# Performance work log

Hardware: AMD Instinct MI355X
Metric: run time of the kernel (lower is better)

Reference implementation:

```python
import jax, jax.numpy as jnp
import numpy as np

BINS = 10

def setup_inputs() -> dict:
    key = jax.random.key(0)
    k1, k2 = jax.random.split(key)
    N, C = 262144, 80
    pred = jax.random.normal(k1, (N, C), dtype=jnp.float32)
    target = jax.random.randint(k2, (N, C), 0, 2, dtype=jnp.int32)
    return {"pred": pred, "target": target}


def _ghmc_loss(pred, target):
    # NOTE: faithful to the original torch code, which applies sigmoid to pred
    # and then feeds that *through binary_cross_entropy_with_logits* (i.e. the
    # sigmoid output is treated as logits -- a double sigmoid quirk we preserve).
    z = jax.nn.sigmoid(pred)                      # [N, C] "logits" fed to BCE-with-logits
    t = target.astype(z.dtype)                    # [N, C]
    # gradient magnitude, detached like pred.detach() in torch
    g = jnp.abs(jax.lax.stop_gradient(z) - t)     # in [0, 1]
    # label_weight is overwritten with ones in the original forward, so every
    # element is valid: tot = N * C.
    tot = jnp.asarray(z.size, dtype=z.dtype)

    # uniform bins: edges[i] = i/BINS, last edge nudged by 1e-6 so g == 1 lands
    # in the last bin -> equivalent to floor(g*BINS) clipped to BINS-1.
    idx = jnp.clip((g * BINS).astype(jnp.int32), 0, BINS - 1)   # [N, C]
    counts = jax.ops.segment_sum(
        jnp.ones((z.size,), dtype=z.dtype), idx.reshape(-1), num_segments=BINS
    )                                                            # [BINS]
    n_nonempty = jnp.sum(counts > 0).astype(z.dtype)
    per_bin_w = jnp.where(counts > 0, tot / jnp.maximum(counts, 1.0), 0.0)  # [BINS]
    weights = per_bin_w[idx] / jnp.maximum(n_nonempty, 1.0)      # [N, C]
    weights = jax.lax.stop_gradient(weights)

    # BCE-with-logits(z, t) = softplus(z) - t*z (numerically stable)
    bce = jax.nn.softplus(z) - t * z
    return jnp.sum(weights * bce) / tot


def reference(pred, target):
    return _ghmc_loss(pred, target)
```

## Files before the change

### kernel.cpp

```cpp
#include <hip/hip_runtime.h>


#define NBINS  10
#define GRID1  2048
#define BLOCK1 256

typedef float vf4 __attribute__((ext_vector_type(4)));
typedef int   vi4 __attribute__((ext_vector_type(4)));

#if __has_builtin(__builtin_amdgcn_exp2f)
__device__ __forceinline__ float nexp2(float a) { return __builtin_amdgcn_exp2f(a); }
#else
__device__ __forceinline__ float nexp2(float a) { return __expf(a * 0.69314718055994531f); }
#endif
#if __has_builtin(__builtin_amdgcn_logf)
__device__ __forceinline__ float nlog2(float a) { return __builtin_amdgcn_logf(a); }
#else
__device__ __forceinline__ float nlog2(float a) { return __logf(a) * 1.44269504088896341f; }
#endif

#define LOG2E 1.44269504088896341f
#define LN2   0.69314718055994531f

#define GLOAD16(gsrc, ldst)                                                \
    __builtin_amdgcn_global_load_lds(                                      \
        (const __attribute__((address_space(1))) void*)(gsrc),             \
        (__attribute__((address_space(3))) void*)(ldst), 16, 0, 0)

__global__ __launch_bounds__(BLOCK1) void ghmc_pass1(
    const vf4* __restrict__ pred4,
    const vi4* __restrict__ targ4,
    float* __restrict__ partial_s,
    int*   __restrict__ partial_c,
    int nvec4)
{
    __shared__ vf4  plds[2][BLOCK1];
    __shared__ vi4  tlds[2][BLOCK1];
    __shared__ float sred[BLOCK1 / 64][NBINS];
    __shared__ int   cred[BLOCK1 / 64][NBINS];

    float s[NBINS];
#pragma unroll
    for (int b = 0; b < NBINS; ++b) s[b] = 0.0f;
    unsigned long long cnt = 0;

    const int tid    = threadIdx.x;
    const int wbase  = tid & ~63;
    const int g0     = blockIdx.x * BLOCK1 + tid;
    const int stride = GRID1 * BLOCK1;
    const int ntiles = nvec4 / stride;

    auto group4 = [&](vf4 p, vi4 t) {
        float z[4], tf[4];
#pragma unroll
        for (int j = 0; j < 4; ++j) {
            tf[j] = (float)t[j];
            z[j]  = __builtin_amdgcn_rcpf(1.0f + nexp2(-p[j] * LOG2E));
        }
        asm volatile("" : "+v"(z[0]), "+v"(z[1]), "+v"(z[2]), "+v"(z[3]));
        int bi[4]; float bce[4];
#pragma unroll
        for (int j = 0; j < 4; ++j) {
            float g = fabsf(z[j] - tf[j]);
            int   b = (int)(g * 10.0f);
            bi[j]   = b > (NBINS - 1) ? (NBINS - 1) : b;
            float sp = nlog2(1.0f + nexp2(z[j] * LOG2E)) * LN2;
            bce[j]  = sp - tf[j] * z[j];
        }
#pragma unroll
        for (int j = 0; j < 4; ++j) {
#pragma unroll
            for (int b = 0; b < NBINS; ++b)
                s[b] += (bi[j] == b) ? bce[j] : 0.0f;
            cnt += 1ull << (6 * bi[j]);
        }
    };

    if (ntiles > 0) {
        GLOAD16(&pred4[g0], &plds[0][wbase]);
        GLOAD16(&targ4[g0], &tlds[0][wbase]);
        __syncthreads();

        int cur = 0;
        for (int t = 0; t < ntiles; ++t) {
            if (t + 1 < ntiles) {
                const int gn = g0 + (t + 1) * stride;
                GLOAD16(&pred4[gn], &plds[cur ^ 1][wbase]);
                GLOAD16(&targ4[gn], &tlds[cur ^ 1][wbase]);
            }
            group4(plds[cur][tid], tlds[cur][tid]);
            __syncthreads();
            cur ^= 1;
        }
    }
    for (int i = g0 + ntiles * stride; i < nvec4; i += stride) {
        vf4 p0 = pred4[i];
        vi4 t0 = targ4[i];
        group4(p0, t0);
    }

    int c[NBINS];
#pragma unroll
    for (int b = 0; b < NBINS; ++b) c[b] = (int)((cnt >> (6 * b)) & 63ull);

#pragma unroll
    for (int b = 0; b < NBINS; ++b) {
#pragma unroll
        for (int off = 32; off > 0; off >>= 1) {
            s[b] += __shfl_down(s[b], off, 64);
            c[b] += __shfl_down(c[b], off, 64);
        }
    }

    const int wave = tid >> 6;
    if ((tid & 63) == 0) {
#pragma unroll
        for (int b = 0; b < NBINS; ++b) { sred[wave][b] = s[b]; cred[wave][b] = c[b]; }
    }
    __syncthreads();
    if (tid < NBINS) {
        int b = tid;
        partial_s[b * GRID1 + blockIdx.x] = sred[0][b] + sred[1][b] + sred[2][b] + sred[3][b];
        partial_c[b * GRID1 + blockIdx.x] = cred[0][b] + cred[1][b] + cred[2][b] + cred[3][b];
    }
}

#define BLOCK2 1024

__global__ __launch_bounds__(BLOCK2) void ghmc_pass2(
    const float* __restrict__ partial_s,
    const int*   __restrict__ partial_c,
    float* __restrict__ out,
    int nblocks)
{
    double as[NBINS];
    int    ac[NBINS];
#pragma unroll
    for (int b = 0; b < NBINS; ++b) { as[b] = 0.0; ac[b] = 0; }

    for (int j = threadIdx.x; j < nblocks; j += BLOCK2) {
#pragma unroll
        for (int b = 0; b < NBINS; ++b) {
            as[b] += (double)partial_s[b * nblocks + j];
            ac[b] += partial_c[b * nblocks + j];
        }
    }

#pragma unroll
    for (int b = 0; b < NBINS; ++b) {
#pragma unroll
        for (int off = 32; off > 0; off >>= 1) {
            as[b] += __shfl_down(as[b], off, 64);
            ac[b] += __shfl_down(ac[b], off, 64);
        }
    }

    __shared__ double sds[BLOCK2 / 64][NBINS];
    __shared__ int    sdc[BLOCK2 / 64][NBINS];
    int wave = threadIdx.x >> 6;
    if ((threadIdx.x & 63) == 0) {
#pragma unroll
        for (int b = 0; b < NBINS; ++b) { sds[wave][b] = as[b]; sdc[wave][b] = ac[b]; }
    }
    __syncthreads();

    if (threadIdx.x == 0) {
        int nn = 0;
        double acc = 0.0;
#pragma unroll
        for (int b = 0; b < NBINS; ++b) {
            double sb = 0.0;
            int    cb = 0;
#pragma unroll
            for (int w = 0; w < BLOCK2 / 64; ++w) { sb += sds[w][b]; cb += sdc[w][b]; }
            if (cb > 0) { nn += 1; acc += sb / (double)cb; }
        }
        out[0] = (float)(acc / (double)(nn > 0 ? nn : 1));
    }
}

extern "C" void kernel_launch(void* const* d_in, const int* in_sizes, int n_in,
                              void* d_out, int out_size, void* d_ws, size_t ws_size,
                              hipStream_t stream)
{
    const float* pred = (const float*)d_in[0];
    const int*   targ = (const int*)d_in[1];
    float*       out  = (float*)d_out;

    const int n     = in_sizes[0];
    const int nvec4 = n / 4;

    float* partial_s = (float*)d_ws;
    int*   partial_c = (int*)((char*)d_ws + GRID1 * NBINS * sizeof(float));

    ghmc_pass1<<<GRID1, BLOCK1, 0, stream>>>(
        (const vf4*)pred, (const vi4*)targ, partial_s, partial_c, nvec4);

    ghmc_pass2<<<1, BLOCK2, 0, stream>>>(partial_s, partial_c, out, GRID1);
}
```

Before: 199.8 us.

## Specialize fully unrolled two-deep LDS prefetch pipeline with explicit waitcnts

Adds a fast path for the case where each thread handles exactly ten tiles. It fully unrolls the loop, issues two tiles of global-to-LDS loads up front, and uses manual vmcnt/lgkmcnt waits with inline ds_read_b128 in place of __syncthreads. Each wave reads only the LDS slots it loaded itself, so block barriers are no longer needed, and the next loads are issued right after the current buffer is read. All other sizes fall back to plain direct global loads. The fast path depends on hard-coded wait counts and on the problem size matching this case exactly.

```diff
diff --git a/kernel.cpp b/kernel.cpp
--- a/kernel.cpp
+++ b/kernel.cpp
@@ -26,6 +26,9 @@
     __builtin_amdgcn_global_load_lds(                                      \
         (const __attribute__((address_space(1))) void*)(gsrc),             \
         (__attribute__((address_space(3))) void*)(ldst), 16, 0, 0)
+
+#define LDSOFF(ptr) ((unsigned)(unsigned long long)                        \
+    (__attribute__((address_space(3))) void*)(ptr))
 
 __global__ __launch_bounds__(BLOCK1) void ghmc_pass1(
     const vf4* __restrict__ pred4,
@@ -76,27 +79,42 @@
         }
     };
 
-    if (ntiles > 0) {
-        GLOAD16(&pred4[g0], &plds[0][wbase]);
-        GLOAD16(&targ4[g0], &tlds[0][wbase]);
-        __syncthreads();
-
-        int cur = 0;
-        for (int t = 0; t < ntiles; ++t) {
-            if (t + 1 < ntiles) {
-                const int gn = g0 + (t + 1) * stride;
-                GLOAD16(&pred4[gn], &plds[cur ^ 1][wbase]);
-                GLOAD16(&targ4[gn], &tlds[cur ^ 1][wbase]);
+    if (ntiles == 10 && nvec4 == 10 * stride) {
+        const unsigned pbase = LDSOFF(&plds[0][0]);
+        const unsigned tbase = LDSOFF(&tlds[0][0]);
+
+        GLOAD16(&pred4[g0],          &plds[0][wbase]);
+        GLOAD16(&targ4[g0],          &tlds[0][wbase]);
+        GLOAD16(&pred4[g0 + stride], &plds[1][wbase]);
+        GLOAD16(&targ4[g0 + stride], &tlds[1][wbase]);
+
+#pragma unroll
+        for (int t = 0; t < 10; ++t) {
+            if (t < 9) asm volatile("s_waitcnt vmcnt(2)" ::: "memory");
+            else       asm volatile("s_waitcnt vmcnt(0)" ::: "memory");
+            __builtin_amdgcn_sched_barrier(0);
+
+            vf4 p; vi4 tt;
+            const unsigned ap = pbase + (unsigned)(((t & 1) * BLOCK1 + tid) * 16);
+            const unsigned at = tbase + (unsigned)(((t & 1) * BLOCK1 + tid) * 16);
+            asm volatile("ds_read_b128 %0, %1" : "=v"(p)  : "v"(ap));
+            asm volatile("ds_read_b128 %0, %1" : "=v"(tt) : "v"(at));
+            asm volatile("s_waitcnt lgkmcnt(0)" ::: "memory");
+            __builtin_amdgcn_sched_barrier(0);
+
+            if (t + 2 < 10) {
+                const int gn = g0 + (t + 2) * stride;
+                GLOAD16(&pred4[gn], &plds[t & 1][wbase]);
+                GLOAD16(&targ4[gn], &tlds[t & 1][wbase]);
             }
-            group4(plds[cur][tid], tlds[cur][tid]);
-            __syncthreads();
-            cur ^= 1;
-        }
-    }
-    for (int i = g0 + ntiles * stride; i < nvec4; i += stride) {
-        vf4 p0 = pred4[i];
-        vi4 t0 = targ4[i];
-        group4(p0, t0);
+            group4(p, tt);
+        }
+    } else {
+        for (int i = g0; i < nvec4; i += stride) {
+            vf4 p0 = pred4[i];
+            vi4 t0 = targ4[i];
+            group4(p0, t0);
+        }
     }
 
     int c[NBINS];
```

Result: no change. 196.3 us (-1.8%).
